# Optimization experiments

Measured on AMD Instinct MI355X. Metric: run time of the kernel, lower is better.

## Reference

```python
import jax, jax.numpy as jnp
import numpy as np
from jax import lax

B, C_IN, H, W = 16, 256, 64, 64
C_OUT, K_SZ, N_EXP, RED_C = 256, 3, 4, 16  # reduction_channels = max(256//16,16)=16


def setup_inputs() -> dict:
    key = jax.random.key(0)
    ks = jax.random.split(key, 6)
    x = jax.random.normal(ks[0], (B, C_IN, H, W), dtype=jnp.float32)
    # routing network params (1x1 convs == dense on pooled features)
    w1 = jax.random.normal(ks[1], (RED_C, C_IN), dtype=jnp.float32) * (1.0 / np.sqrt(C_IN))
    b1 = jnp.zeros((RED_C,), dtype=jnp.float32)
    w2 = jax.random.normal(ks[2], (N_EXP * C_IN, RED_C), dtype=jnp.float32) * (1.0 / np.sqrt(RED_C))
    b2 = jnp.zeros((N_EXP * C_IN,), dtype=jnp.float32)
    # expert weight bank (num_experts, c_out, c_in, kh, kw)
    fan_in = C_IN * K_SZ * K_SZ
    bound = np.sqrt(6.0 / fan_in)  # kaiming_uniform with a=sqrt(5) ~ U(-sqrt(6/fan_in)*..., simplified scale)
    weight = jax.random.uniform(ks[3], (N_EXP, C_OUT, C_IN, K_SZ, K_SZ), dtype=jnp.float32, minval=-bound, maxval=bound)
    return {"x": x, "w1": w1, "b1": b1, "w2": w2, "b2": b2, "weight": weight}


def reference(x, w1, b1, w2, b2, weight):
    b = x.shape[0]
    # route_func: global avg pool -> 1x1 conv -> relu -> 1x1 conv -> sigmoid
    pooled = jnp.mean(x, axis=(2, 3))                       # (b, c_in)
    r = jax.nn.relu(pooled @ w1.T + b1)                     # (b, red_c)
    rw = jax.nn.sigmoid(r @ w2.T + b2)                      # (b, K*c_in)
    rw = rw.reshape(b, N_EXP, C_IN)                         # (b, K, c_in)
    # per-sample combined kernel: sum over experts, routing scales input channels
    combined = jnp.einsum('bkc,kocij->bocij', rw, weight)   # (b, c_out, c_in, kh, kw)
    # per-sample conv (equivalent to groups=b trick in torch)
    def conv_one(xi, wi):
        return lax.conv_general_dilated(
            xi[None], wi, window_strides=(1, 1), padding=[(1, 1), (1, 1)],
            dimension_numbers=('NCHW', 'OIHW', 'NCHW'))[0]
    out = jax.vmap(conv_one)(x, combined)                   # (b, c_out, h, w)
    return out
```

## Files before the change

### kernel.cpp

```cpp
#include <hip/hip_runtime.h>
#include <hip/hip_bf16.h>
#include <math.h>

#define BB   16
#define CIN  256
#define HH   64
#define WW   64
#define COUT 256
#define NEXP 4
#define REDC 16
#define HW   (HH*WW)

typedef __attribute__((ext_vector_type(8))) short short8;
typedef __attribute__((ext_vector_type(16))) float f32x16;

#define AS1 __attribute__((address_space(1)))
#define AS3 __attribute__((address_space(3)))

__device__ __forceinline__ void gld_lds16(void* lds, const void* gp) {
    __builtin_amdgcn_global_load_lds((const AS1 unsigned int*)gp,
                                     (AS3 unsigned int*)lds, 16, 0, 0);
}

__global__ __launch_bounds__(256)
void transpose_pool_kernel(const float* __restrict__ x, ushort* __restrict__ xT,
                           float* __restrict__ pp) {
    int blk = blockIdx.x;
    int sq = blk & 3;
    int chunk = (blk >> 2) & 7;
    int b = blk >> 5;
    int c0 = chunk * 32;
    int s0 = sq * 1024;
    int tid = threadIdx.x;
    const float* xb = x + ((size_t)(b * CIN + c0)) * HW;

    float psum[32];
    #pragma unroll
    for (int i = 0; i < 32; ++i) psum[i] = 0.f;

    for (int it = 0; it < 4; ++it) {
        int s = s0 + it * 256 + tid;
        unsigned int pk[16];
        #pragma unroll
        for (int p = 0; p < 16; ++p) {
            float lo = xb[(size_t)(2 * p) * HW + s];
            float hi = xb[(size_t)(2 * p + 1) * HW + s];
            psum[2 * p]     += lo;
            psum[2 * p + 1] += hi;
            asm volatile("v_cvt_pk_bf16_f32 %0, %1, %2" : "=v"(pk[p]) : "v"(lo), "v"(hi));
        }
        #pragma unroll
        for (int q = 0; q < 4; ++q) {
            ushort* dst = xT + ((size_t)(b * 32 + chunk * 4 + q) * HW + s) * 8;
            *(uint4*)dst = make_uint4(pk[q * 4], pk[q * 4 + 1], pk[q * 4 + 2], pk[q * 4 + 3]);
        }
    }

    __shared__ float red[4][32];
    int lane = tid & 63, wid = tid >> 6;
    #pragma unroll
    for (int i = 0; i < 32; ++i) {
        float v = psum[i];
        #pragma unroll
        for (int off = 32; off > 0; off >>= 1) v += __shfl_down(v, off, 64);
        if (lane == 0) red[wid][i] = v;
    }
    __syncthreads();
    if (tid < 32)
        pp[(b * 4 + sq) * 256 + c0 + tid] = red[0][tid] + red[1][tid] + red[2][tid] + red[3][tid];
}

__global__ void route_kernel(const float* __restrict__ pp,
                             const float* __restrict__ w1, const float* __restrict__ b1,
                             const float* __restrict__ w2, const float* __restrict__ b2,
                             float* __restrict__ rw) {
    __shared__ float p_s[BB][CIN];
    __shared__ float r_s[BB][REDC];
    int tid = threadIdx.x;
    for (int i = tid; i < BB * CIN; i += 256) {
        int b = i >> 8, c = i & 255;
        p_s[b][c] = (pp[(b * 4 + 0) * 256 + c] + pp[(b * 4 + 1) * 256 + c] +
                     pp[(b * 4 + 2) * 256 + c] + pp[(b * 4 + 3) * 256 + c]) * (1.0f / HW);
    }
    __syncthreads();
    {
        int b = tid >> 4, j = tid & 15;
        float acc = b1[j];
        for (int c = 0; c < CIN; ++c) acc += p_s[b][c] * w1[j * CIN + c];
        r_s[b][j] = fmaxf(acc, 0.f);
    }
    __syncthreads();
    for (int i = tid; i < BB * NEXP * CIN; i += 256) {
        int b = i >> 10, o2 = i & 1023;
        float acc = b2[o2];
        #pragma unroll
        for (int j = 0; j < REDC; ++j) acc += r_s[b][j] * w2[o2 * REDC + j];
        rw[i] = 1.f / (1.f + expf(-acc));
    }
}

__global__ __launch_bounds__(256)
void combine3_kernel(const float* __restrict__ rw,
                     const float* __restrict__ weight,
                     ushort* __restrict__ cw) {
    int blk = blockIdx.x;
    int u = blk >> 1;
    int t = (blk & 1) * 256 + threadIdx.x;
    int gg = u & 1;
    int v = u >> 1;
    int t9 = v % 9;
    int cu = v / 9;
    int chunk16 = cu & 15;
    int ot = cu >> 4;
    int o_loc = t >> 3, c8 = t & 7;
    int o = ot * 64 + o_loc;
    int c = chunk16 * 16 + gg * 8 + c8;

    __shared__ float rw_s[16][4][8];
    int tid = threadIdx.x;
    #pragma unroll
    for (int r = 0; r < 2; ++r) {
        int i = r * 256 + tid;
        if (i < 512) {
            int b = i >> 5, k = (i >> 3) & 3, cc = i & 7;
            rw_s[b][k][cc] = rw[b * 1024 + k * 256 + chunk16 * 16 + gg * 8 + cc];
        }
    }
    __syncthreads();

    float wk0 = weight[((size_t)(0 * COUT + o) * CIN + c) * 9 + t9];
    float wk1 = weight[((size_t)(1 * COUT + o) * CIN + c) * 9 + t9];
    float wk2 = weight[((size_t)(2 * COUT + o) * CIN + c) * 9 + t9];
    float wk3 = weight[((size_t)(3 * COUT + o) * CIN + c) * 9 + t9];

    size_t base = (size_t)u * 512 + t;
    #pragma unroll
    for (int b = 0; b < 16; ++b) {
        float acc = rw_s[b][0][c8] * wk0 + rw_s[b][1][c8] * wk1 +
                    rw_s[b][2][c8] * wk2 + rw_s[b][3][c8] * wk3;
        __hip_bfloat16 hv = __float2bfloat16(acc);
        cw[base + (size_t)b * 589824] = *(ushort*)&hv;
    }
}

__global__ __launch_bounds__(256, 2)
void conv_mfma(const ushort* __restrict__ xT, const ushort* __restrict__ cw,
               float* __restrict__ out, const ushort* __restrict__ zp) {
    __shared__ char LDS[2][40576];

    int blk = blockIdx.x;
    int L = (blk & 7) * 64 + (blk >> 3);
    int b  = L >> 5;
    int rt = (L >> 2) & 7;
    int ot = L & 3;
    int r0 = rt * 8, o0 = ot * 64;
    int tid = threadIdx.x;
    int lane = tid & 63, wid = tid >> 6;
    int l31 = lane & 31, h = lane >> 5;

    f32x16 acc[2][4];
    #pragma unroll
    for (int mi = 0; mi < 2; ++mi)
        #pragma unroll
        for (int f = 0; f < 4; ++f) acc[mi][f] = (f32x16)0.f;

    const char* xTb = (const char*)(xT + (size_t)b * 32 * HW * 8);
    const ushort* Ab = cw + (size_t)((b * 4 + ot) * 16) * 9216;

    const char* srcb[10];
    int dsto[10];
    int strd[10];
    #pragma unroll
    for (int i = 0; i < 10; ++i) {
        int u = wid * 10 + i;
        if (u < 18) {
            srcb[i] = (const char*)(Ab + (size_t)u * 512) + lane * 16;
            dsto[i] = u * 1024;
            strd[i] = 18432;
        } else if (u < 38) {
            int ux = u - 18;
            int r = ux >> 1, half = ux & 1;
            int grow = r0 - 1 + r;
            bool valid = (grow >= 0 && grow < 64);
            srcb[i] = valid
                ? xTb + (size_t)(half * HW + grow * 64) * 16 + lane * 16
                : (const char*)zp + lane * 16;
            dsto[i] = 18432 + (half * 660 + r * 66 + 1) * 16;
            strd[i] = valid ? 131072 : 0;
        } else {
            srcb[i] = (const char*)zp + lane * 16;
            dsto[i] = 39552;
            strd[i] = 0;
        }
    }

    char* ldsb = &LDS[0][0];

    for (int i = tid; i < 20288; i += 256) ((unsigned int*)ldsb)[i] = 0;
    __syncthreads();

    #define STAGE(BUF, CH)                                                    \
    {                                                                         \
        _Pragma("unroll")                                                     \
        for (int i = 0; i < 10; ++i)                                          \
            gld_lds16(ldsb + (BUF) * 40576 + dsto[i],                         \
                      srcb[i] + (size_t)(CH) * strd[i]);                      \
    }

    #define LDA(T, pa, pb)                                                    \
        pa = *(const short8*)&asb[(((T) * 2 + h) * 64 + 0  + l31) * 8];       \
        pb = *(const short8*)&asb[(((T) * 2 + h) * 64 + 32 + l31) * 8];

    #define LDB(R, S, DJ, v)                                                  \
        v = *(const short8*)&xsb[((wid * 2 + (R)) * 66 + (S) * 32 + l31 + (DJ)) * 8];

    #define DO4(pa, pb, v0, v1, v2, v3)                                                \
    {                                                                                  \
        acc[0][0] = __builtin_amdgcn_mfma_f32_32x32x16_bf16(pa, v0, acc[0][0], 0,0,0); \
        acc[1][0] = __builtin_amdgcn_mfma_f32_32x32x16_bf16(pb, v0, acc[1][0], 0,0,0); \
        acc[0][1] = __builtin_amdgcn_mfma_f32_32x32x16_bf16(pa, v1, acc[0][1], 0,0,0); \
        acc[1][1] = __builtin_amdgcn_mfma_f32_32x32x16_bf16(pb, v1, acc[1][1], 0,0,0); \
        acc[0][2] = __builtin_amdgcn_mfma_f32_32x32x16_bf16(pa, v2, acc[0][2], 0,0,0); \
        acc[1][2] = __builtin_amdgcn_mfma_f32_32x32x16_bf16(pb, v2, acc[1][2], 0,0,0); \
        acc[0][3] = __builtin_amdgcn_mfma_f32_32x32x16_bf16(pa, v3, acc[0][3], 0,0,0); \
        acc[1][3] = __builtin_amdgcn_mfma_f32_32x32x16_bf16(pb, v3, acc[1][3], 0,0,0); \
    }

    #define GROUP(DJ)                                                         \
    {                                                                         \
        short8 x00, x01, x10, x11, x20, x21, x30, x31, pa, pb, qa, qb;        \
        LDB(0, 0, DJ, x00) LDB(0, 1, DJ, x01)                                 \
        LDB(1, 0, DJ, x10) LDB(1, 1, DJ, x11)                                 \
        LDA(DJ, pa, pb)                                                       \
        LDB(2, 0, DJ, x20) LDB(2, 1, DJ, x21)                                 \
        LDA((DJ) + 3, qa, qb)                                                 \
        DO4(pa, pb, x00, x01, x10, x11)                           \
        LDB(3, 0, DJ, x30) LDB(3, 1, DJ, x31)                                 \
        LDA((DJ) + 6, pa, pb)                                                 \
        DO4(qa, qb, x10, x11, x20, x21)                           \
        DO4(pa, pb, x20, x21, x30, x31)                           \
    }

    STAGE(0, 0)

    #pragma unroll 1
    for (int chunk = 0; chunk < 16; ++chunk) {
        int cur = chunk & 1;
        if (chunk < 15) {
            STAGE(cur ^ 1, chunk + 1)
            asm volatile("s_waitcnt vmcnt(10)" ::: "memory");
        } else {
            asm volatile("s_waitcnt vmcnt(0)" ::: "memory");
        }
        __builtin_amdgcn_s_barrier();

        const ushort* asb = (const ushort*)(ldsb + cur * 40576);
        const ushort* xsb = (const ushort*)(ldsb + cur * 40576 + 18432) + h * 5280;

        __builtin_amdgcn_s_setprio(1);
        GROUP(0)
        GROUP(1)
        GROUP(2)
        __builtin_amdgcn_s_setprio(0);

        __builtin_amdgcn_s_barrier();
    }

    #pragma unroll
    for (int mi = 0; mi < 2; ++mi) {
        #pragma unroll
        for (int f = 0; f < 4; ++f) {
            int pos = (r0 + wid * 2 + (f >> 1)) * 64 + (f & 1) * 32 + l31;
            #pragma unroll
            for (int j = 0; j < 16; ++j) {
                int orow = (j & 3) + 8 * (j >> 2) + 4 * h;
                out[((size_t)(b * COUT + o0 + mi * 32 + orow)) * HW + pos] = acc[mi][f][j];
            }
        }
    }
    #undef STAGE
    #undef LDA
    #undef LDB
    #undef DO4
    #undef GROUP
}

extern "C" void kernel_launch(void* const* d_in, const int* in_sizes, int n_in,
                              void* d_out, int out_size, void* d_ws, size_t ws_size,
                              hipStream_t stream) {
    const float* x      = (const float*)d_in[0];
    const float* w1     = (const float*)d_in[1];
    const float* b1     = (const float*)d_in[2];
    const float* w2     = (const float*)d_in[3];
    const float* b2     = (const float*)d_in[4];
    const float* weight = (const float*)d_in[5];
    float* out = (float*)d_out;

    float*  ws = (float*)d_ws;
    float*  pp = ws;
    float*  rw = ws + 16384;
    ushort* cw = (ushort*)(ws + 32768);
    ushort* xT = (ushort*)(ws + 32768 + 4718592);
    ushort* zp = xT + 16777216;

    hipMemsetAsync(zp, 0, 2048, stream);
    transpose_pool_kernel<<<512, 256, 0, stream>>>(x, xT, pp);
    route_kernel<<<1, 256, 0, stream>>>(pp, w1, b1, w2, b2, rw);
    combine3_kernel<<<2304, 256, 0, stream>>>(rw, weight, cw);
    conv_mfma<<<512, 256, 0, stream>>>(xT, cw, out, zp);
}
```

Measured before the change: 142.0 us.

## Halve conv tile rows, drop LDS double buffering, raise occupancy to 4 blocks

```diff
diff --git a/kernel.cpp b/kernel.cpp
--- a/kernel.cpp
+++ b/kernel.cpp
@@ -143,41 +143,40 @@
     }
 }
 
-__global__ __launch_bounds__(256, 2)
+__global__ __launch_bounds__(256, 4)
 void conv_mfma(const ushort* __restrict__ xT, const ushort* __restrict__ cw,
                float* __restrict__ out, const ushort* __restrict__ zp) {
-    __shared__ char LDS[2][40576];
+    __shared__ char LDS[32128];
 
     int blk = blockIdx.x;
-    int L = (blk & 7) * 64 + (blk >> 3);
-    int b  = L >> 5;
-    int rt = (L >> 2) & 7;
+    int L = (blk & 7) * 128 + (blk >> 3);
+    int b  = L >> 6;
+    int rt = (L >> 2) & 15;
     int ot = L & 3;
-    int r0 = rt * 8, o0 = ot * 64;
+    int r0 = rt * 4, o0 = ot * 64;
     int tid = threadIdx.x;
     int lane = tid & 63, wid = tid >> 6;
     int l31 = lane & 31, h = lane >> 5;
-
-    f32x16 acc[2][4];
-    #pragma unroll
-    for (int mi = 0; mi < 2; ++mi)
-        #pragma unroll
-        for (int f = 0; f < 4; ++f) acc[mi][f] = (f32x16)0.f;
+    int og = wid & 1, rg = wid >> 1;
+
+    f32x16 acc[4];
+    #pragma unroll
+    for (int f = 0; f < 4; ++f) acc[f] = (f32x16)0.f;
 
     const char* xTb = (const char*)(xT + (size_t)b * 32 * HW * 8);
     const ushort* Ab = cw + (size_t)((b * 4 + ot) * 16) * 9216;
 
-    const char* srcb[10];
-    int dsto[10];
-    int strd[10];
-    #pragma unroll
-    for (int i = 0; i < 10; ++i) {
-        int u = wid * 10 + i;
+    const char* srcb[8];
+    int dsto[8];
+    int strd[8];
+    #pragma unroll
+    for (int i = 0; i < 8; ++i) {
+        int u = wid * 8 + i;
         if (u < 18) {
             srcb[i] = (const char*)(Ab + (size_t)u * 512) + lane * 16;
             dsto[i] = u * 1024;
             strd[i] = 18432;
-        } else if (u < 38) {
+        } else if (u < 30) {
             int ux = u - 18;
             int r = ux >> 1, half = ux & 1;
             int grow = r0 - 1 + r;
@@ -185,97 +184,76 @@
             srcb[i] = valid
                 ? xTb + (size_t)(half * HW + grow * 64) * 16 + lane * 16
                 : (const char*)zp + lane * 16;
-            dsto[i] = 18432 + (half * 660 + r * 66 + 1) * 16;
+            dsto[i] = 18432 + (half * 396 + r * 66 + 1) * 16;
             strd[i] = valid ? 131072 : 0;
         } else {
             srcb[i] = (const char*)zp + lane * 16;
-            dsto[i] = 39552;
+            dsto[i] = 31104;
             strd[i] = 0;
         }
     }
 
-    char* ldsb = &LDS[0][0];
-
-    for (int i = tid; i < 20288; i += 256) ((unsigned int*)ldsb)[i] = 0;
-    __syncthreads();
-
-    #define STAGE(BUF, CH)                                                    \
+    for (int i = tid; i < 8032; i += 256) ((unsigned int*)LDS)[i] = 0;
+    __syncthreads();
+
+    #define STAGE(CH)                                                         \
     {                                                                         \
         _Pragma("unroll")                                                     \
-        for (int i = 0; i < 10; ++i)                                          \
-            gld_lds16(ldsb + (BUF) * 40576 + dsto[i],                         \
-                      srcb[i] + (size_t)(CH) * strd[i]);                      \
-    }
-
-    #define LDA(T, pa, pb)                                                    \
-        pa = *(const short8*)&asb[(((T) * 2 + h) * 64 + 0  + l31) * 8];       \
-        pb = *(const short8*)&asb[(((T) * 2 + h) * 64 + 32 + l31) * 8];
+        for (int i = 0; i < 8; ++i)                                           \
+            gld_lds16(LDS + dsto[i], srcb[i] + (size_t)(CH) * strd[i]);       \
+    }
+
+    #define LDA(T, pa)                                                        \
+        pa = *(const short8*)&asb[(((T) * 2 + h) * 64 + og * 32 + l31) * 8];
 
     #define LDB(R, S, DJ, v)                                                  \
-        v = *(const short8*)&xsb[((wid * 2 + (R)) * 66 + (S) * 32 + l31 + (DJ)) * 8];
-
-    #define DO4(pa, pb, v0, v1, v2, v3)                                                \
-    {                                                                                  \
-        acc[0][0] = __builtin_amdgcn_mfma_f32_32x32x16_bf16(pa, v0, acc[0][0], 0,0,0); \
-        acc[1][0] = __builtin_amdgcn_mfma_f32_32x32x16_bf16(pb, v0, acc[1][0], 0,0,0); \
-        acc[0][1] = __builtin_amdgcn_mfma_f32_32x32x16_bf16(pa, v1, acc[0][1], 0,0,0); \
-        acc[1][1] = __builtin_amdgcn_mfma_f32_32x32x16_bf16(pb, v1, acc[1][1], 0,0,0); \
-        acc[0][2] = __builtin_amdgcn_mfma_f32_32x32x16_bf16(pa, v2, acc[0][2], 0,0,0); \
-        acc[1][2] = __builtin_amdgcn_mfma_f32_32x32x16_bf16(pb, v2, acc[1][2], 0,0,0); \
-        acc[0][3] = __builtin_amdgcn_mfma_f32_32x32x16_bf16(pa, v3, acc[0][3], 0,0,0); \
-        acc[1][3] = __builtin_amdgcn_mfma_f32_32x32x16_bf16(pb, v3, acc[1][3], 0,0,0); \
+        v = *(const short8*)&xsb[((rg * 2 + (R)) * 66 + (S) * 32 + l31 + (DJ)) * 8];
+
+    #define DO4(pa, v0, v1, v2, v3)                                                   \
+    {                                                                                 \
+        acc[0] = __builtin_amdgcn_mfma_f32_32x32x16_bf16(pa, v0, acc[0], 0, 0, 0);    \
+        acc[1] = __builtin_amdgcn_mfma_f32_32x32x16_bf16(pa, v1, acc[1], 0, 0, 0);    \
+        acc[2] = __builtin_amdgcn_mfma_f32_32x32x16_bf16(pa, v2, acc[2], 0, 0, 0);    \
+        acc[3] = __builtin_amdgcn_mfma_f32_32x32x16_bf16(pa, v3, acc[3], 0, 0, 0);    \
     }
 
     #define GROUP(DJ)                                                         \
     {                                                                         \
-        short8 x00, x01, x10, x11, x20, x21, x30, x31, pa, pb, qa, qb;        \
+        short8 x00, x01, x10, x11, x20, x21, x30, x31, pa, qa, ra;            \
         LDB(0, 0, DJ, x00) LDB(0, 1, DJ, x01)                                 \
         LDB(1, 0, DJ, x10) LDB(1, 1, DJ, x11)                                 \
-        LDA(DJ, pa, pb)                                                       \
+        LDA(DJ, pa)                                                           \
         LDB(2, 0, DJ, x20) LDB(2, 1, DJ, x21)                                 \
-        LDA((DJ) + 3, qa, qb)                                                 \
-        DO4(pa, pb, x00, x01, x10, x11)                           \
+        LDA((DJ) + 3, qa)                                                     \
+        DO4(pa, x00, x01, x10, x11)                               \
         LDB(3, 0, DJ, x30) LDB(3, 1, DJ, x31)                                 \
-        LDA((DJ) + 6, pa, pb)                                                 \
-        DO4(qa, qb, x10, x11, x20, x21)                           \
-        DO4(pa, pb, x20, x21, x30, x31)                           \
-    }
-
-    STAGE(0, 0)
+        LDA((DJ) + 6, ra)                                                     \
+        DO4(qa, x10, x11, x20, x21)                               \
+        DO4(ra, x20, x21, x30, x31)                               \
+    }
 
     #pragma unroll 1
     for (int chunk = 0; chunk < 16; ++chunk) {
-        int cur = chunk & 1;
-        if (chunk < 15) {
-            STAGE(cur ^ 1, chunk + 1)
-            asm volatile("s_waitcnt vmcnt(10)" ::: "memory");
-        } else {
-            asm volatile("s_waitcnt vmcnt(0)" ::: "memory");
-        }
-        __builtin_amdgcn_s_barrier();
-
-        const ushort* asb = (const ushort*)(ldsb + cur * 40576);
-        const ushort* xsb = (const ushort*)(ldsb + cur * 40576 + 18432) + h * 5280;
-
-        __builtin_amdgcn_s_setprio(1);
+        STAGE(chunk)
+        __syncthreads();
+
+        const ushort* asb = (const ushort*)LDS;
+        const ushort* xsb = (const ushort*)(LDS + 18432) + h * 3168;
+
         GROUP(0)
         GROUP(1)
         GROUP(2)
-        __builtin_amdgcn_s_setprio(0);
-
-        __builtin_amdgcn_s_barrier();
-    }
-
-    #pragma unroll
-    for (int mi = 0; mi < 2; ++mi) {
-        #pragma unroll
-        for (int f = 0; f < 4; ++f) {
-            int pos = (r0 + wid * 2 + (f >> 1)) * 64 + (f & 1) * 32 + l31;
-            #pragma unroll
-            for (int j = 0; j < 16; ++j) {
-                int orow = (j & 3) + 8 * (j >> 2) + 4 * h;
-                out[((size_t)(b * COUT + o0 + mi * 32 + orow)) * HW + pos] = acc[mi][f][j];
-            }
+
+        __syncthreads();
+    }
+
+    #pragma unroll
+    for (int f = 0; f < 4; ++f) {
+        int pos = (r0 + rg * 2 + (f >> 1)) * 64 + (f & 1) * 32 + l31;
+        #pragma unroll
+        for (int j = 0; j < 16; ++j) {
+            int orow = (j & 3) + 8 * (j >> 2) + 4 * h;
+            out[((size_t)(b * COUT + o0 + og * 32 + orow)) * HW + pos] = acc[f][j];
         }
     }
     #undef STAGE
@@ -307,5 +285,5 @@
     transpose_pool_kernel<<<512, 256, 0, stream>>>(x, xT, pp);
     route_kernel<<<1, 256, 0, stream>>>(pp, w1, b1, w2, b2, rw);
     combine3_kernel<<<2304, 256, 0, stream>>>(rw, weight, cw);
-    conv_mfma<<<512, 256, 0, stream>>>(xT, cw, out, zp);
-}
+    conv_mfma<<<1024, 256, 0, stream>>>(xT, cw, out, zp);
+}
```

After: 146.8 us. 1.03x slower.
